# Optimization experiments

Hardware: AMD Instinct MI355X
Metric: run time of the kernel (lower is better)

## Reference

```python
import jax, jax.numpy as jnp
import numpy as np

# Config constants (match init_kwargs)
THR = 0.2
TEMPERATURE = 0.1
BORDER_RM = 2
H0C, W0C = 60, 80  # L = 4800
H1C, W1C = 60, 80  # S = 4800


def setup_inputs() -> dict:
    key = jax.random.key(0)
    k0, k1 = jax.random.split(key)
    feat_c0 = jax.random.normal(k0, (2, 4800, 256), dtype=jnp.float32)
    feat_c1 = jax.random.normal(k1, (2, 4800, 256), dtype=jnp.float32)
    return {"feat_c0": feat_c0, "feat_c1": feat_c1}


def _border_mask_1d(h, w, b):
    """Flattened [h*w] bool mask that is False within b of any border."""
    ih = jnp.arange(h)
    iw = jnp.arange(w)
    mh = (ih >= b) & (ih < h - b)
    mw = (iw >= b) & (iw < w - b)
    return (mh[:, None] & mw[None, :]).reshape(-1)


def reference(feat_c0, feat_c1):
    N, L, C = feat_c0.shape
    # Normalize features and compute similarity (dual-softmax)
    scale = 1.0 / (C ** 0.5)
    sim = jnp.einsum('nlc,nsc->nls', feat_c0 * scale, feat_c1 * scale) / TEMPERATURE
    conf = jax.nn.softmax(sim, axis=1) * jax.nn.softmax(sim, axis=2)  # [N, L, S]

    # Threshold + border removal (mask_border path, no padding masks)
    bm0 = _border_mask_1d(H0C, W0C, BORDER_RM)  # [L]
    bm1 = _border_mask_1d(H1C, W1C, BORDER_RM)  # [S]
    mask = (conf > THR) & bm0[None, :, None] & bm1[None, None, :]

    # Mutual nearest neighbor
    mask = mask \
        & (conf == jnp.max(conf, axis=2, keepdims=True)) \
        & (conf == jnp.max(conf, axis=1, keepdims=True))

    # Per-row match: j index of the (at most one) surviving entry, and its conf.
    # Fixed-shape analogue of torch.where extraction: mconf==0 means no match.
    mask_v = jnp.any(mask, axis=2)                         # [N, L]
    j_ids = jnp.argmax(mask, axis=2)                       # [N, L]
    mconf = jnp.take_along_axis(conf, j_ids[..., None], axis=2)[..., 0]
    mconf = jnp.where(mask_v, mconf, 0.0)                  # [N, L]

    return conf, mask_v, j_ids, mconf
```

## Files before the change

### kernel.cpp

```cpp
#include <hip/hip_runtime.h>
#include <hip/hip_bf16.h>
#include <cstdint>

#define L_DIM 4800
#define C_DIM 256
#define CONF_ELEMS ((size_t)2 * L_DIM * L_DIM)

typedef _Float16 f16x8 __attribute__((ext_vector_type(8)));
typedef float f32x4 __attribute__((ext_vector_type(4)));

typedef const __attribute__((address_space(1))) uint32_t glb_u32;
typedef __attribute__((address_space(3))) uint32_t lds_u32;

#define WS_F16_NEEDED 15705600

__global__ __launch_bounds__(256) void k_cvt2(const float* __restrict__ f0,
                                              const float* __restrict__ f1,
                                              _Float16* __restrict__ h0,
                                              _Float16* __restrict__ h1) {
    int b = blockIdx.x;
    const float* src = (b < 1200) ? f0 : f1;
    _Float16* dst = (b < 1200) ? h0 : h1;
    int i = (b < 1200 ? b : b - 1200) * 256 + threadIdx.x;
    const float4* s4 = (const float4*)src;
    float4 a = s4[(size_t)i * 2], c = s4[(size_t)i * 2 + 1];
    f16x8 h = { (_Float16)a.x, (_Float16)a.y, (_Float16)a.z, (_Float16)a.w,
                (_Float16)c.x, (_Float16)c.y, (_Float16)c.z, (_Float16)c.w };
    *(f16x8*)(dst + (size_t)i * 8) = h;
}

__global__ __launch_bounds__(256) void k_reduceA(const float* __restrict__ partA,
                                                 float* __restrict__ invsum) {
    int i = blockIdx.x * 256 + threadIdx.x;
    if (i >= 19200) return;
    int base = (i < 9600) ? 0 : 50;
    int j = (i < 9600) ? i : i - 9600;
    float s = 0.f;
#pragma unroll 10
    for (int k = 0; k < 50; ++k)
        s += partA[(size_t)(base + k) * 9600 + j];
    invsum[i] = 1.0f / s;
}

__global__ __launch_bounds__(256) void k_reduceB(const unsigned* __restrict__ colbest,
                                                 unsigned* __restrict__ colmaxF) {
    int i = blockIdx.x * 256 + threadIdx.x;
    if (i >= 9600) return;
    unsigned m = 0u;
#pragma unroll 10
    for (int k = 0; k < 50; ++k)
        m = max(m, colbest[(size_t)k * 9600 + i]);
    colmaxF[i] = m;
}

template<bool F16SRC, bool FINAL>
__global__ __launch_bounds__(256) void k_gemm2(const void* __restrict__ srcA,
                                               const void* __restrict__ srcB,
                                               float* __restrict__ conf,
                                               const float* __restrict__ invsum,
                                               float* __restrict__ partA,
                                               unsigned long long* __restrict__ rowbest,
                                               unsigned* __restrict__ colbest) {
    const int xcd = blockIdx.x & 7;
    const int idx = blockIdx.x >> 3;
    const int t   = xcd * 625 + idx;
    const int n   = t / 2500;
    const int rem = t - n * 2500;
    const int ty  = rem / 50;
    const int tx  = rem - ty * 50;
    const int l0  = ty * 96;
    const int s0  = tx * 96;

    __shared__ __align__(16) _Float16 As[2][96 * 64];
    __shared__ __align__(16) _Float16 Bs[2][96 * 64];
    __shared__ __align__(16) char redbuf[2304];

    const int tid  = threadIdx.x;
    const int lane = tid & 63;
    const int w    = tid >> 6;
    const int wr   = w >> 1, wc = w & 1;
    const int q    = lane >> 4, r16 = lane & 15;

    f32x4 acc[3][3] = {};

    const _Float16* Ah = (const _Float16*)srcA + ((size_t)n * L_DIM + l0) * C_DIM;
    const _Float16* Bh = (const _Float16*)srcB + ((size_t)n * L_DIM + s0) * C_DIM;
    const float*    Af = (const float*)srcA + ((size_t)n * L_DIM + l0) * C_DIM;
    const float*    Bf = (const float*)srcB + ((size_t)n * L_DIM + s0) * C_DIM;

    auto stage = [&](int kt, int buf) {
        const int k0 = kt * 64;
        if constexpr (F16SRC) {
#pragma unroll
            for (int i = 0; i < 3; ++i) {
                int c   = tid + i * 256;
                int row = c >> 3;
                int kc  = (c & 7) ^ (row & 7);
                __builtin_amdgcn_global_load_lds(
                    (glb_u32*)(Ah + (size_t)row * C_DIM + k0 + kc * 8),
                    (lds_u32*)(&As[buf][(i * 256 + w * 64) * 8]), 16, 0, 0);
                __builtin_amdgcn_global_load_lds(
                    (glb_u32*)(Bh + (size_t)row * C_DIM + k0 + kc * 8),
                    (lds_u32*)(&Bs[buf][(i * 256 + w * 64) * 8]), 16, 0, 0);
            }
        } else {
#pragma unroll
            for (int i = 0; i < 3; ++i) {
                int c   = tid + i * 256;
                int row = c >> 3;
                int kc  = (c & 7) ^ (row & 7);
                const float* pa = Af + (size_t)row * C_DIM + k0 + kc * 8;
                const float* pb = Bf + (size_t)row * C_DIM + k0 + kc * 8;
                float4 a0 = ((const float4*)pa)[0], a1 = ((const float4*)pa)[1];
                float4 b0 = ((const float4*)pb)[0], b1 = ((const float4*)pb)[1];
                f16x8 ha = { (_Float16)a0.x, (_Float16)a0.y, (_Float16)a0.z, (_Float16)a0.w,
                             (_Float16)a1.x, (_Float16)a1.y, (_Float16)a1.z, (_Float16)a1.w };
                f16x8 hb = { (_Float16)b0.x, (_Float16)b0.y, (_Float16)b0.z, (_Float16)b0.w,
                             (_Float16)b1.x, (_Float16)b1.y, (_Float16)b1.z, (_Float16)b1.w };
                *(f16x8*)(&As[buf][(size_t)c * 8]) = ha;
                *(f16x8*)(&Bs[buf][(size_t)c * 8]) = hb;
            }
        }
    };

    auto compute = [&](int buf) {
        f16x8 af[2][3], bf[2][3];
#pragma unroll
        for (int m = 0; m < 3; ++m) {
            int row = wr * 48 + m * 16 + r16;
#pragma unroll
            for (int ks = 0; ks < 2; ++ks)
                af[ks][m] = *(const f16x8*)(&As[buf][row * 64 + (((ks * 4 + q) ^ (row & 7)) * 8)]);
        }
#pragma unroll
        for (int nn = 0; nn < 3; ++nn) {
            int row = wc * 48 + nn * 16 + r16;
#pragma unroll
            for (int ks = 0; ks < 2; ++ks)
                bf[ks][nn] = *(const f16x8*)(&Bs[buf][row * 64 + (((ks * 4 + q) ^ (row & 7)) * 8)]);
        }
#pragma unroll
        for (int ks = 0; ks < 2; ++ks)
#pragma unroll
            for (int m = 0; m < 3; ++m)
#pragma unroll
                for (int nn = 0; nn < 3; ++nn)
                    acc[m][nn] = __builtin_amdgcn_mfma_f32_16x16x32_f16(af[ks][m], bf[ks][nn], acc[m][nn], 0, 0, 0);
    };

    stage(0, 0);
    __syncthreads();
#pragma unroll
    for (int kt = 0; kt < 4; ++kt) {
        if (kt < 3) stage(kt + 1, (kt + 1) & 1);
        compute(kt & 1);
        __syncthreads();
    }

    const float SIM_SCALE = 0.0390625f;

    if constexpr (!FINAL) {
        float* redR = (float*)redbuf;
        float* redC = (float*)(redbuf + 768);
        float cp[3] = {0.f, 0.f, 0.f};
#pragma unroll
        for (int m = 0; m < 3; ++m) {
#pragma unroll
            for (int reg = 0; reg < 4; ++reg) {
                float rsum = 0.f;
#pragma unroll
                for (int nn = 0; nn < 3; ++nn) {
                    float e = __expf(acc[m][nn][reg] * SIM_SCALE);
                    rsum += e;
                    cp[nn] += e;
                }
                rsum += __shfl_xor(rsum, 1);
                rsum += __shfl_xor(rsum, 2);
                rsum += __shfl_xor(rsum, 4);
                rsum += __shfl_xor(rsum, 8);
                if (r16 == 0)
                    redR[wc * 96 + wr * 48 + m * 16 + q * 4 + reg] = rsum;
            }
        }
#pragma unroll
        for (int nn = 0; nn < 3; ++nn) {
            float v = cp[nn];
            v += __shfl_xor(v, 16);
            v += __shfl_xor(v, 32);
            if (q == 0)
                redC[wr * 96 + wc * 48 + nn * 16 + r16] = v;
        }
        __syncthreads();
        if (tid < 96) {
            partA[(size_t)tx * 9600 + n * L_DIM + l0 + tid] = redR[tid] + redR[96 + tid];
        } else if (tid < 192) {
            int c = tid - 96;
            partA[(size_t)(50 + ty) * 9600 + n * L_DIM + s0 + c] = redC[c] + redC[96 + c];
        }
    } else {
        unsigned long long* redRB = (unsigned long long*)redbuf;
        unsigned* redCB = (unsigned*)(redbuf + 1536);
        const size_t base = (size_t)n * L_DIM * L_DIM;
        float ivC[3];
#pragma unroll
        for (int nn = 0; nn < 3; ++nn)
            ivC[nn] = invsum[9600 + n * L_DIM + s0 + wc * 48 + nn * 16 + r16];
        float cmx[3] = {0.f, 0.f, 0.f};
#pragma unroll
        for (int m = 0; m < 3; ++m) {
#pragma unroll
            for (int reg = 0; reg < 4; ++reg) {
                const int grow = l0 + wr * 48 + m * 16 + q * 4 + reg;
                const float ivR = invsum[n * L_DIM + grow];
                const size_t rowoff = base + (size_t)grow * L_DIM;
                float bv = -1.f; int bc = 0;
#pragma unroll
                for (int nn = 0; nn < 3; ++nn) {
                    const int gcol = s0 + wc * 48 + nn * 16 + r16;
                    float cf = __expf(acc[m][nn][reg] * (2.0f * SIM_SCALE)) * ivR * ivC[nn];
                    conf[rowoff + gcol] = cf;
                    cmx[nn] = fmaxf(cmx[nn], cf);
                    if (cf > bv) { bv = cf; bc = gcol; }
                }
                unsigned long long pack =
                    ((unsigned long long)__float_as_uint(bv) << 32) |
                    (unsigned long long)(0xFFFFFFFFu - (unsigned)bc);
#pragma unroll
                for (int d = 1; d < 16; d <<= 1) {
                    unsigned long long o = __shfl_xor(pack, d);
                    if (o > pack) pack = o;
                }
                if (r16 == 0)
                    redRB[wc * 96 + wr * 48 + m * 16 + q * 4 + reg] = pack;
            }
        }
#pragma unroll
        for (int nn = 0; nn < 3; ++nn) {
            float v = cmx[nn];
            v = fmaxf(v, __shfl_xor(v, 16));
            v = fmaxf(v, __shfl_xor(v, 32));
            if (q == 0)
                redCB[wr * 96 + wc * 48 + nn * 16 + r16] = __float_as_uint(v);
        }
        __syncthreads();
        if (tid < 96) {
            unsigned long long p0 = redRB[tid], p1 = redRB[96 + tid];
            rowbest[(size_t)tx * 9600 + n * L_DIM + l0 + tid] = (p0 > p1) ? p0 : p1;
        } else if (tid < 192) {
            int c = tid - 96;
            colbest[(size_t)ty * 9600 + n * L_DIM + s0 + c] = max(redCB[c], redCB[96 + c]);
        }
    }
}

__global__ __launch_bounds__(256) void k_match(const unsigned long long* __restrict__ rowbest,
                                               const unsigned* __restrict__ colmaxF,
                                               float* __restrict__ out) {
    int i = blockIdx.x * 256 + threadIdx.x;
    if (i >= 2 * L_DIM) return;
    unsigned long long p = 0ull;
#pragma unroll 10
    for (int k = 0; k < 50; ++k) {
        unsigned long long o = rowbest[(size_t)k * 9600 + i];
        if (o > p) p = o;
    }
    int n = i / L_DIM, l = i % L_DIM;
    float v = __uint_as_float((unsigned)(p >> 32));
    int cand = (int)(0xFFFFFFFFu - (unsigned)(p & 0xFFFFFFFFull));
    if (cand < 0 || cand >= L_DIM) cand = 0;
    int h0 = l / 80, w0 = l % 80;
    int h1 = cand / 80, w1 = cand % 80;
    bool bm0 = (h0 >= 2) && (h0 < 58) && (w0 >= 2) && (w0 < 78);
    bool bm1 = (h1 >= 2) && (h1 < 58) && (w1 >= 2) && (w1 < 78);
    float cm = __uint_as_float(colmaxF[n * L_DIM + cand]);
    bool mask = (v > 0.2f) && bm0 && bm1 && (v == cm);
    out[CONF_ELEMS + i]         = mask ? 1.0f : 0.0f;
    out[CONF_ELEMS + 9600 + i]  = mask ? (float)cand : 0.0f;
    out[CONF_ELEMS + 19200 + i] = mask ? v : 0.0f;
}

extern "C" void kernel_launch(void* const* d_in, const int* in_sizes, int n_in,
                              void* d_out, int out_size, void* d_ws, size_t ws_size,
                              hipStream_t stream) {
    const float* f0 = (const float*)d_in[0];
    const float* f1 = (const float*)d_in[1];
    float* out = (float*)d_out;

    float* invsum = (float*)d_ws;
    unsigned* colmaxF = (unsigned*)((char*)d_ws + 76800);
    float* partA = (float*)((char*)d_ws + 115200);
    unsigned long long* rowbest = (unsigned long long*)((char*)d_ws + 115200);
    unsigned* colbest = (unsigned*)((char*)d_ws + 3955200);
    _Float16* h0 = (_Float16*)((char*)d_ws + 5875200);
    _Float16* h1 = h0 + (size_t)2 * L_DIM * C_DIM;

    const bool usef16 = ws_size >= WS_F16_NEEDED;

    if (usef16) {
        k_cvt2<<<dim3(2400), 256, 0, stream>>>(f0, f1, h0, h1);
        k_gemm2<true, false><<<dim3(5000), 256, 0, stream>>>(
            h0, h1, out, invsum, partA, rowbest, colbest);
        k_reduceA<<<dim3(75), 256, 0, stream>>>(partA, invsum);
        k_gemm2<true, true><<<dim3(5000), 256, 0, stream>>>(
            h0, h1, out, invsum, partA, rowbest, colbest);
    } else {
        k_gemm2<false, false><<<dim3(5000), 256, 0, stream>>>(
            f0, f1, out, invsum, partA, rowbest, colbest);
        k_reduceA<<<dim3(75), 256, 0, stream>>>(partA, invsum);
        k_gemm2<false, true><<<dim3(5000), 256, 0, stream>>>(
            f0, f1, out, invsum, partA, rowbest, colbest);
    }
    k_reduceB<<<dim3(38), 256, 0, stream>>>(colbest, colmaxF);
    k_match<<<dim3(38), 256, 0, stream>>>(rowbest, colmaxF, out);
}
```

Measured before the change: 147.3 us.

## Enlarge GEMM tiles to 192x192 with 32x32 MFMA and single-buffered LDS

Tiles grow from 96x96 to 192x192 per block, so there are a quarter as many blocks and partial-reduction slabs. The inner product switches from 16x16x32 to 32x32x16 MFMA, giving each wave a 96x96 output. Double buffering is dropped in favour of a single LDS buffer with syncs around each k-step, and row inverse sums are cached in LDS. The larger tiles are meant to cut global operand reloads and the size of the partial reductions, at the cost of losing load/compute overlap, higher register pressure from 144 accumulator floats per lane, and a tail effect with only 1250 blocks.

New measurement: 148.7 us. No clear change (+0.9%).

```diff
diff --git a/kernel.cpp b/kernel.cpp
--- a/kernel.cpp
+++ b/kernel.cpp
@@ -8,11 +8,12 @@
 
 typedef _Float16 f16x8 __attribute__((ext_vector_type(8)));
 typedef float f32x4 __attribute__((ext_vector_type(4)));
+typedef float f32x16 __attribute__((ext_vector_type(16)));
 
 typedef const __attribute__((address_space(1))) uint32_t glb_u32;
 typedef __attribute__((address_space(3))) uint32_t lds_u32;
 
-#define WS_F16_NEEDED 15705600
+#define WS_F16_NEEDED 12825600
 
 __global__ __launch_bounds__(256) void k_cvt2(const float* __restrict__ f0,
                                               const float* __restrict__ f1,
@@ -33,11 +34,11 @@
                                                  float* __restrict__ invsum) {
     int i = blockIdx.x * 256 + threadIdx.x;
     if (i >= 19200) return;
-    int base = (i < 9600) ? 0 : 50;
+    int base = (i < 9600) ? 0 : 25;
     int j = (i < 9600) ? i : i - 9600;
     float s = 0.f;
-#pragma unroll 10
-    for (int k = 0; k < 50; ++k)
+#pragma unroll 5
+    for (int k = 0; k < 25; ++k)
         s += partA[(size_t)(base + k) * 9600 + j];
     invsum[i] = 1.0f / s;
 }
@@ -47,65 +48,73 @@
     int i = blockIdx.x * 256 + threadIdx.x;
     if (i >= 9600) return;
     unsigned m = 0u;
-#pragma unroll 10
-    for (int k = 0; k < 50; ++k)
+#pragma unroll 5
+    for (int k = 0; k < 25; ++k)
         m = max(m, colbest[(size_t)k * 9600 + i]);
     colmaxF[i] = m;
 }
 
 template<bool F16SRC, bool FINAL>
-__global__ __launch_bounds__(256) void k_gemm2(const void* __restrict__ srcA,
-                                               const void* __restrict__ srcB,
-                                               float* __restrict__ conf,
-                                               const float* __restrict__ invsum,
-                                               float* __restrict__ partA,
-                                               unsigned long long* __restrict__ rowbest,
-                                               unsigned* __restrict__ colbest) {
-    const int xcd = blockIdx.x & 7;
-    const int idx = blockIdx.x >> 3;
-    const int t   = xcd * 625 + idx;
-    const int n   = t / 2500;
-    const int rem = t - n * 2500;
-    const int ty  = rem / 50;
-    const int tx  = rem - ty * 50;
-    const int l0  = ty * 96;
-    const int s0  = tx * 96;
-
-    __shared__ __align__(16) _Float16 As[2][96 * 64];
-    __shared__ __align__(16) _Float16 Bs[2][96 * 64];
-    __shared__ __align__(16) char redbuf[2304];
+__global__ __launch_bounds__(256, 2) void k_gemm2(const void* __restrict__ srcA,
+                                                  const void* __restrict__ srcB,
+                                                  float* __restrict__ conf,
+                                                  const float* __restrict__ invsum,
+                                                  float* __restrict__ partA,
+                                                  unsigned long long* __restrict__ rowbest,
+                                                  unsigned* __restrict__ colbest) {
+    const int orig = blockIdx.x;
+    const int xcd  = orig & 7;
+    const int q8   = 156, r8 = 2;
+    const int t    = (xcd < r8 ? xcd * (q8 + 1) : r8 * (q8 + 1) + (xcd - r8) * q8) + (orig >> 3);
+    const int n    = t / 625;
+    const int rem  = t - n * 625;
+    const int ty   = rem / 25;
+    const int tx   = rem - ty * 25;
+    const int l0   = ty * 192;
+    const int s0   = tx * 192;
+
+    __shared__ __align__(16) _Float16 As[192 * 64];
+    __shared__ __align__(16) _Float16 Bs[192 * 64];
+    __shared__ __align__(16) char redbuf[4608];
+    __shared__ float ivr_lds[192];
 
     const int tid  = threadIdx.x;
     const int lane = tid & 63;
     const int w    = tid >> 6;
     const int wr   = w >> 1, wc = w & 1;
-    const int q    = lane >> 4, r16 = lane & 15;
-
-    f32x4 acc[3][3] = {};
+    const int l31  = lane & 31;
+    const int hi   = lane >> 5;
+
+    if constexpr (FINAL) {
+        if (tid < 192) ivr_lds[tid] = invsum[n * L_DIM + l0 + tid];
+    }
+
+    f32x16 acc[3][3] = {};
 
     const _Float16* Ah = (const _Float16*)srcA + ((size_t)n * L_DIM + l0) * C_DIM;
     const _Float16* Bh = (const _Float16*)srcB + ((size_t)n * L_DIM + s0) * C_DIM;
     const float*    Af = (const float*)srcA + ((size_t)n * L_DIM + l0) * C_DIM;
     const float*    Bf = (const float*)srcB + ((size_t)n * L_DIM + s0) * C_DIM;
 
-    auto stage = [&](int kt, int buf) {
+    for (int kt = 0; kt < 4; ++kt) {
         const int k0 = kt * 64;
+        __syncthreads();
         if constexpr (F16SRC) {
 #pragma unroll
-            for (int i = 0; i < 3; ++i) {
+            for (int i = 0; i < 6; ++i) {
                 int c   = tid + i * 256;
                 int row = c >> 3;
                 int kc  = (c & 7) ^ (row & 7);
                 __builtin_amdgcn_global_load_lds(
                     (glb_u32*)(Ah + (size_t)row * C_DIM + k0 + kc * 8),
-                    (lds_u32*)(&As[buf][(i * 256 + w * 64) * 8]), 16, 0, 0);
+                    (lds_u32*)(As + (i * 256 + w * 64) * 8), 16, 0, 0);
                 __builtin_amdgcn_global_load_lds(
                     (glb_u32*)(Bh + (size_t)row * C_DIM + k0 + kc * 8),
-                    (lds_u32*)(&Bs[buf][(i * 256 + w * 64) * 8]), 16, 0, 0);
+                    (lds_u32*)(Bs + (i * 256 + w * 64) * 8), 16, 0, 0);
             }
         } else {
 #pragma unroll
-            for (int i = 0; i < 3; ++i) {
+            for (int i = 0; i < 6; ++i) {
                 int c   = tid + i * 256;
                 int row = c >> 3;
                 int kc  = (c & 7) ^ (row & 7);
@@ -117,138 +126,122 @@
                              (_Float16)a1.x, (_Float16)a1.y, (_Float16)a1.z, (_Float16)a1.w };
                 f16x8 hb = { (_Float16)b0.x, (_Float16)b0.y, (_Float16)b0.z, (_Float16)b0.w,
                              (_Float16)b1.x, (_Float16)b1.y, (_Float16)b1.z, (_Float16)b1.w };
-                *(f16x8*)(&As[buf][(size_t)c * 8]) = ha;
-                *(f16x8*)(&Bs[buf][(size_t)c * 8]) = hb;
-            }
-        }
-    };
-
-    auto compute = [&](int buf) {
-        f16x8 af[2][3], bf[2][3];
-#pragma unroll
-        for (int m = 0; m < 3; ++m) {
-            int row = wr * 48 + m * 16 + r16;
-#pragma unroll
-            for (int ks = 0; ks < 2; ++ks)
-                af[ks][m] = *(const f16x8*)(&As[buf][row * 64 + (((ks * 4 + q) ^ (row & 7)) * 8)]);
-        }
-#pragma unroll
-        for (int nn = 0; nn < 3; ++nn) {
-            int row = wc * 48 + nn * 16 + r16;
-#pragma unroll
-            for (int ks = 0; ks < 2; ++ks)
-                bf[ks][nn] = *(const f16x8*)(&Bs[buf][row * 64 + (((ks * 4 + q) ^ (row & 7)) * 8)]);
-        }
-#pragma unroll
-        for (int ks = 0; ks < 2; ++ks)
-#pragma unroll
-            for (int m = 0; m < 3; ++m)
-#pragma unroll
-                for (int nn = 0; nn < 3; ++nn)
-                    acc[m][nn] = __builtin_amdgcn_mfma_f32_16x16x32_f16(af[ks][m], bf[ks][nn], acc[m][nn], 0, 0, 0);
-    };
-
-    stage(0, 0);
-    __syncthreads();
-#pragma unroll
-    for (int kt = 0; kt < 4; ++kt) {
-        if (kt < 3) stage(kt + 1, (kt + 1) & 1);
-        compute(kt & 1);
+                *(f16x8*)(As + (size_t)c * 8) = ha;
+                *(f16x8*)(Bs + (size_t)c * 8) = hb;
+            }
+        }
         __syncthreads();
+
+#pragma unroll
+        for (int ks = 0; ks < 4; ++ks) {
+            f16x8 af[3], bf[3];
+#pragma unroll
+            for (int mi = 0; mi < 3; ++mi) {
+                int row = wr * 96 + mi * 32 + l31;
+                int ck  = (ks * 2 + hi) ^ (row & 7);
+                af[mi] = *(const f16x8*)(As + row * 64 + ck * 8);
+            }
+#pragma unroll
+            for (int ni = 0; ni < 3; ++ni) {
+                int row = wc * 96 + ni * 32 + l31;
+                int ck  = (ks * 2 + hi) ^ (row & 7);
+                bf[ni] = *(const f16x8*)(Bs + row * 64 + ck * 8);
+            }
+#pragma unroll
+            for (int mi = 0; mi < 3; ++mi)
+#pragma unroll
+                for (int ni = 0; ni < 3; ++ni)
+                    acc[mi][ni] = __builtin_amdgcn_mfma_f32_32x32x16_f16(af[mi], bf[ni], acc[mi][ni], 0, 0, 0);
+        }
     }
 
     const float SIM_SCALE = 0.0390625f;
 
     if constexpr (!FINAL) {
         float* redR = (float*)redbuf;
-        float* redC = (float*)(redbuf + 768);
+        float* redC = (float*)(redbuf + 1536);
         float cp[3] = {0.f, 0.f, 0.f};
 #pragma unroll
-        for (int m = 0; m < 3; ++m) {
-#pragma unroll
-            for (int reg = 0; reg < 4; ++reg) {
-                float rsum = 0.f;
-#pragma unroll
-                for (int nn = 0; nn < 3; ++nn) {
-                    float e = __expf(acc[m][nn][reg] * SIM_SCALE);
-                    rsum += e;
-                    cp[nn] += e;
-                }
+        for (int mi = 0; mi < 3; ++mi) {
+#pragma unroll
+            for (int reg = 0; reg < 16; ++reg) {
+                float e0 = __expf(acc[mi][0][reg] * SIM_SCALE);
+                float e1 = __expf(acc[mi][1][reg] * SIM_SCALE);
+                float e2 = __expf(acc[mi][2][reg] * SIM_SCALE);
+                cp[0] += e0; cp[1] += e1; cp[2] += e2;
+                float rsum = e0 + e1 + e2;
                 rsum += __shfl_xor(rsum, 1);
                 rsum += __shfl_xor(rsum, 2);
                 rsum += __shfl_xor(rsum, 4);
                 rsum += __shfl_xor(rsum, 8);
-                if (r16 == 0)
-                    redR[wc * 96 + wr * 48 + m * 16 + q * 4 + reg] = rsum;
-            }
-        }
-#pragma unroll
-        for (int nn = 0; nn < 3; ++nn) {
-            float v = cp[nn];
-            v += __shfl_xor(v, 16);
+                rsum += __shfl_xor(rsum, 16);
+                if (l31 == 0) {
+                    int rl = wr * 96 + mi * 32 + (reg & 3) + 8 * (reg >> 2) + 4 * hi;
+                    redR[wc * 192 + rl] = rsum;
+                }
+            }
+        }
+#pragma unroll
+        for (int ni = 0; ni < 3; ++ni) {
+            float v = cp[ni];
             v += __shfl_xor(v, 32);
-            if (q == 0)
-                redC[wr * 96 + wc * 48 + nn * 16 + r16] = v;
+            if (hi == 0)
+                redC[wr * 192 + wc * 96 + ni * 32 + l31] = v;
         }
         __syncthreads();
-        if (tid < 96) {
-            partA[(size_t)tx * 9600 + n * L_DIM + l0 + tid] = redR[tid] + redR[96 + tid];
-        } else if (tid < 192) {
-            int c = tid - 96;
-            partA[(size_t)(50 + ty) * 9600 + n * L_DIM + s0 + c] = redC[c] + redC[96 + c];
+        if (tid < 192) {
+            partA[(size_t)tx * 9600 + n * L_DIM + l0 + tid] = redR[tid] + redR[192 + tid];
+            partA[(size_t)(25 + ty) * 9600 + n * L_DIM + s0 + tid] = redC[tid] + redC[192 + tid];
         }
     } else {
         unsigned long long* redRB = (unsigned long long*)redbuf;
-        unsigned* redCB = (unsigned*)(redbuf + 1536);
+        unsigned* redCB = (unsigned*)(redbuf + 3072);
         const size_t base = (size_t)n * L_DIM * L_DIM;
         float ivC[3];
 #pragma unroll
-        for (int nn = 0; nn < 3; ++nn)
-            ivC[nn] = invsum[9600 + n * L_DIM + s0 + wc * 48 + nn * 16 + r16];
+        for (int ni = 0; ni < 3; ++ni)
+            ivC[ni] = invsum[9600 + n * L_DIM + s0 + wc * 96 + ni * 32 + l31];
         float cmx[3] = {0.f, 0.f, 0.f};
 #pragma unroll
-        for (int m = 0; m < 3; ++m) {
-#pragma unroll
-            for (int reg = 0; reg < 4; ++reg) {
-                const int grow = l0 + wr * 48 + m * 16 + q * 4 + reg;
-                const float ivR = invsum[n * L_DIM + grow];
-                const size_t rowoff = base + (size_t)grow * L_DIM;
+        for (int mi = 0; mi < 3; ++mi) {
+#pragma unroll
+            for (int reg = 0; reg < 16; ++reg) {
+                const int rl   = wr * 96 + mi * 32 + (reg & 3) + 8 * (reg >> 2) + 4 * hi;
+                const float ivR = ivr_lds[rl];
+                const size_t rowoff = base + (size_t)(l0 + rl) * L_DIM;
                 float bv = -1.f; int bc = 0;
 #pragma unroll
-                for (int nn = 0; nn < 3; ++nn) {
-                    const int gcol = s0 + wc * 48 + nn * 16 + r16;
-                    float cf = __expf(acc[m][nn][reg] * (2.0f * SIM_SCALE)) * ivR * ivC[nn];
+                for (int ni = 0; ni < 3; ++ni) {
+                    const int gcol = s0 + wc * 96 + ni * 32 + l31;
+                    float cf = __expf(acc[mi][ni][reg] * (2.0f * SIM_SCALE)) * ivR * ivC[ni];
                     conf[rowoff + gcol] = cf;
-                    cmx[nn] = fmaxf(cmx[nn], cf);
+                    cmx[ni] = fmaxf(cmx[ni], cf);
                     if (cf > bv) { bv = cf; bc = gcol; }
                 }
                 unsigned long long pack =
                     ((unsigned long long)__float_as_uint(bv) << 32) |
                     (unsigned long long)(0xFFFFFFFFu - (unsigned)bc);
 #pragma unroll
-                for (int d = 1; d < 16; d <<= 1) {
+                for (int d = 1; d < 32; d <<= 1) {
                     unsigned long long o = __shfl_xor(pack, d);
                     if (o > pack) pack = o;
                 }
-                if (r16 == 0)
-                    redRB[wc * 96 + wr * 48 + m * 16 + q * 4 + reg] = pack;
-            }
-        }
-#pragma unroll
-        for (int nn = 0; nn < 3; ++nn) {
-            float v = cmx[nn];
-            v = fmaxf(v, __shfl_xor(v, 16));
+                if (l31 == 0)
+                    redRB[wc * 192 + rl] = pack;
+            }
+        }
+#pragma unroll
+        for (int ni = 0; ni < 3; ++ni) {
+            float v = cmx[ni];
             v = fmaxf(v, __shfl_xor(v, 32));
-            if (q == 0)
-                redCB[wr * 96 + wc * 48 + nn * 16 + r16] = __float_as_uint(v);
+            if (hi == 0)
+                redCB[wr * 192 + wc * 96 + ni * 32 + l31] = __float_as_uint(v);
         }
         __syncthreads();
-        if (tid < 96) {
-            unsigned long long p0 = redRB[tid], p1 = redRB[96 + tid];
+        if (tid < 192) {
+            unsigned long long p0 = redRB[tid], p1 = redRB[192 + tid];
             rowbest[(size_t)tx * 9600 + n * L_DIM + l0 + tid] = (p0 > p1) ? p0 : p1;
-        } else if (tid < 192) {
-            int c = tid - 96;
-            colbest[(size_t)ty * 9600 + n * L_DIM + s0 + c] = max(redCB[c], redCB[96 + c]);
+            colbest[(size_t)ty * 9600 + n * L_DIM + s0 + tid] = max(redCB[tid], redCB[192 + tid]);
         }
     }
 }
@@ -259,8 +252,8 @@
     int i = blockIdx.x * 256 + threadIdx.x;
     if (i >= 2 * L_DIM) return;
     unsigned long long p = 0ull;
-#pragma unroll 10
-    for (int k = 0; k < 50; ++k) {
+#pragma unroll 5
+    for (int k = 0; k < 25; ++k) {
         unsigned long long o = rowbest[(size_t)k * 9600 + i];
         if (o > p) p = o;
     }
@@ -290,24 +283,24 @@
     unsigned* colmaxF = (unsigned*)((char*)d_ws + 76800);
     float* partA = (float*)((char*)d_ws + 115200);
     unsigned long long* rowbest = (unsigned long long*)((char*)d_ws + 115200);
-    unsigned* colbest = (unsigned*)((char*)d_ws + 3955200);
-    _Float16* h0 = (_Float16*)((char*)d_ws + 5875200);
+    unsigned* colbest = (unsigned*)((char*)d_ws + 2035200);
+    _Float16* h0 = (_Float16*)((char*)d_ws + 2995200);
     _Float16* h1 = h0 + (size_t)2 * L_DIM * C_DIM;
 
     const bool usef16 = ws_size >= WS_F16_NEEDED;
 
     if (usef16) {
         k_cvt2<<<dim3(2400), 256, 0, stream>>>(f0, f1, h0, h1);
-        k_gemm2<true, false><<<dim3(5000), 256, 0, stream>>>(
+        k_gemm2<true, false><<<dim3(1250), 256, 0, stream>>>(
             h0, h1, out, invsum, partA, rowbest, colbest);
         k_reduceA<<<dim3(75), 256, 0, stream>>>(partA, invsum);
-        k_gemm2<true, true><<<dim3(5000), 256, 0, stream>>>(
+        k_gemm2<true, true><<<dim3(1250), 256, 0, stream>>>(
             h0, h1, out, invsum, partA, rowbest, colbest);
     } else {
-        k_gemm2<false, false><<<dim3(5000), 256, 0, stream>>>(
+        k_gemm2<false, false><<<dim3(1250), 256, 0, stream>>>(
             f0, f1, out, invsum, partA, rowbest, colbest);
         k_reduceA<<<dim3(75), 256, 0, stream>>>(partA, invsum);
-        k_gemm2<false, true><<<dim3(5000), 256, 0, stream>>>(
+        k_gemm2<false, true><<<dim3(1250), 256, 0, stream>>>(
             f0, f1, out, invsum, partA, rowbest, colbest);
     }
     k_reduceB<<<dim3(38), 256, 0, stream>>>(colbest, colmaxF);
```
